# Performance work log

Hardware: AMD Instinct MI355X
Metric: run time of the kernel (lower is better)

## Reference

```python
import jax, jax.numpy as jnp
import numpy as np

B, T = 64, 4096
K = 67            # 25 body + 21 + 21 hand keypoints
D = 256           # first_layer_size
C = 7             # num_classes
THR = 0.1         # confidence_threshold
EPS = 1e-5        # BatchNorm eps


def setup_inputs() -> dict:
    key = jax.random.key(0)
    ks = jax.random.split(key, 8)
    body = jax.random.normal(ks[0], (B, T, 75), dtype=jnp.float32)
    hand_right = jax.random.normal(ks[1], (B, T, 63), dtype=jnp.float32)
    hand_left = jax.random.normal(ks[2], (B, T, 63), dtype=jnp.float32)
    length = jax.random.randint(ks[3], (B,), 1, T + 1, dtype=jnp.int64)
    W1 = jax.random.normal(ks[4], (2 * K, D), dtype=jnp.float32) * 0.05
    b1 = jnp.zeros((D,), dtype=jnp.float32)
    gamma = jnp.ones((D,), dtype=jnp.float32)
    beta = jnp.zeros((D,), dtype=jnp.float32)
    Wc = jax.random.normal(ks[5], (D, C), dtype=jnp.float32) * 0.05
    bc = jnp.zeros((C,), dtype=jnp.float32)
    return {"body": body, "hand_right": hand_right, "hand_left": hand_left,
            "length": length, "W1": W1, "b1": b1, "gamma": gamma,
            "beta": beta, "Wc": Wc, "bc": bc}


def reference(body, hand_right, hand_left, length, W1, b1, gamma, beta, Wc, bc):
    # concat keypoint streams -> [B, T, 3K] -> [B, T, K, 3]
    feats = jnp.concatenate([body, hand_right, hand_left], axis=2)
    feats = feats.reshape(feats.shape[0], feats.shape[1], -1, 3)
    x, y, conf = feats[..., 0], feats[..., 1], feats[..., 2]
    conf = (conf > THR).astype(feats.dtype)
    # gate coords by confidence, flatten to [B, T, 2K]
    pos = jnp.stack([x * conf, y * conf], axis=3)
    pos = pos.reshape(pos.shape[0], pos.shape[1], -1)
    # static MLP: Linear + ReLU -> [B, T, D]
    sf = jax.nn.relu(jnp.einsum("btf,fd->btd", pos, W1) + b1)
    # masked max pool over valid timesteps (vectorized segment-max)
    mask = jnp.arange(sf.shape[1])[None, :] < length[:, None]      # [B, T]
    pooled = jnp.max(jnp.where(mask[:, :, None], sf, -jnp.inf), axis=1)  # [B, D]
    # BatchNorm1d (training mode: batch statistics)
    mean = pooled.mean(axis=0)
    var = pooled.var(axis=0)
    bn = (pooled - mean) / jnp.sqrt(var + EPS) * gamma + beta
    # classifier
    return bn @ Wc + bc
```

## Files before the change

### kernel.cpp

```cpp
#include <hip/hip_runtime.h>
#include <hip/hip_bf16.h>

#define B_   64
#define T_   4096
#define K_   67
#define F_   134
#define FP_  160
#define D_   256
#define C_   7
#define THR_ 0.1f
#define EPS_ 1e-5f

typedef __bf16 bf16x8 __attribute__((ext_vector_type(8)));
typedef float  f32x4  __attribute__((ext_vector_type(4)));


__device__ __forceinline__ int a_idx(int t, int f) {
    return (((t >> 4) * 5 + (f >> 5)) * 512) +
           ((((f >> 3) & 3) * 16 + (t & 15)) * 8) + (f & 7);
}

__device__ __forceinline__ int get_len(const int* L, int b) {
    return (L[1] == 0) ? L[2 * b] : L[b];
}

__global__ void convert_w1(const float* __restrict__ W1, __bf16* __restrict__ W1bf) {
    int idx = blockIdx.x * 256 + threadIdx.x;
    if (idx < F_ * D_) {
        int f = idx >> 8, d = idx & 255;
        W1bf[d * FP_ + f] = (__bf16)W1[idx];
    } else if (idx < D_ * FP_) {
        int i2 = idx - F_ * D_;
        int d = i2 / 26, f = F_ + i2 % 26;
        W1bf[d * FP_ + f] = (__bf16)0.f;
    }
}

__device__ __forceinline__ void stage_triple(const float* p, int t, int kglob,
                                             __bf16* As) {
    float x = p[0], y = p[1], cf = p[2];
    if (!(cf > THR_)) { x = 0.f; y = 0.f; }
    unsigned short ux = __builtin_bit_cast(unsigned short, (__bf16)x);
    unsigned short uy = __builtin_bit_cast(unsigned short, (__bf16)y);
    int idx = a_idx(t, 2 * kglob);
    *(unsigned int*)((unsigned short*)As + idx) =
        (unsigned int)ux | ((unsigned int)uy << 16);
}

__global__ __launch_bounds__(256, 3)
void fused_mlp_pool(const float* __restrict__ body,
                    const float* __restrict__ hr,
                    const float* __restrict__ hl,
                    const int*   __restrict__ length,
                    const float* __restrict__ b1,
                    const __bf16* __restrict__ W1bf,
                    float* __restrict__ pooled)
{
    const int b = blockIdx.y;
    const int len = get_len(length, b);
    const int cbase = blockIdx.x * 128;
    if (cbase >= len) return;

    __shared__ __align__(16) __bf16 As[2 * 5 * 512];

    const int tid  = threadIdx.x;
    const int wave = tid >> 6;
    const int lane = tid & 63;
    const int quad = lane >> 4;
    const int l16  = lane & 15;
    const int dbase = wave * 64;

    for (int i = tid; i < 32 * 13; i += 256) {
        int t = i / 13;
        int f = 134 + 2 * (i % 13);
        *(unsigned int*)((unsigned short*)As + a_idx(t, f)) = 0u;
    }

    bf16x8 bfrag[4][5];
    float  b1v[4];
#pragma unroll
    for (int n = 0; n < 4; n++) {
        int d = dbase + n * 16 + l16;
        const __bf16* p = W1bf + d * FP_ + quad * 8;
#pragma unroll
        for (int kt = 0; kt < 5; kt++)
            bfrag[n][kt] = *(const bf16x8*)(p + kt * 32);
        b1v[n] = b1[d];
    }

    float runmax[4] = {0.f, 0.f, 0.f, 0.f};
    const long rowb = (long)b * T_;

    for (int c = 0; c < 4; c++) {
        const int t0 = cbase + c * 32;
        if (t0 >= len) break;
        if (c) __syncthreads();

        const float* bodyt = body + (rowb + t0) * 75;
        for (int j = tid; j < 32 * 25; j += 256) {
            int t = j / 25, k = j - t * 25;
            stage_triple(bodyt + t * 75 + k * 3, t, k, As);
        }
        const float* hrt = hr + (rowb + t0) * 63;
        for (int j = tid; j < 32 * 21; j += 256) {
            int t = j / 21, k = j - t * 21;
            stage_triple(hrt + t * 63 + k * 3, t, 25 + k, As);
        }
        const float* hlt = hl + (rowb + t0) * 63;
        for (int j = tid; j < 32 * 21; j += 256) {
            int t = j / 21, k = j - t * 21;
            stage_triple(hlt + t * 63 + k * 3, t, 46 + k, As);
        }
        __syncthreads();

        f32x4 acc[2][4];
#pragma unroll
        for (int m = 0; m < 2; m++)
#pragma unroll
            for (int n = 0; n < 4; n++)
                acc[m][n] = (f32x4){0.f, 0.f, 0.f, 0.f};

#pragma unroll
        for (int kt = 0; kt < 5; kt++) {
            bf16x8 a0 = *(const bf16x8*)(As + (0 * 5 + kt) * 512 + lane * 8);
            bf16x8 a1 = *(const bf16x8*)(As + (1 * 5 + kt) * 512 + lane * 8);
#pragma unroll
            for (int n = 0; n < 4; n++) {
                acc[0][n] = __builtin_amdgcn_mfma_f32_16x16x32_bf16(a0, bfrag[n][kt], acc[0][n], 0, 0, 0);
                acc[1][n] = __builtin_amdgcn_mfma_f32_16x16x32_bf16(a1, bfrag[n][kt], acc[1][n], 0, 0, 0);
            }
        }

#pragma unroll
        for (int m = 0; m < 2; m++) {
            int trow0 = t0 + m * 16 + quad * 4;
#pragma unroll
            for (int r = 0; r < 4; r++) {
                bool valid = (trow0 + r) < len;
#pragma unroll
                for (int n = 0; n < 4; n++) {
                    float v = acc[m][n][r] + b1v[n];
                    v = (v > 0.f) ? v : 0.f;
                    runmax[n] = (valid && v > runmax[n]) ? v : runmax[n];
                }
            }
        }
    }

#pragma unroll
    for (int n = 0; n < 4; n++) {
        float r = runmax[n];
        r = fmaxf(r, __shfl_xor(r, 16, 64));
        r = fmaxf(r, __shfl_xor(r, 32, 64));
        if (quad == n) {
            atomicMax((unsigned int*)(pooled + b * D_ + dbase + n * 16 + l16),
                      __float_as_uint(r));
        }
    }
}

__global__ void bn_classifier(const float* __restrict__ pooled,
                              const float* __restrict__ gamma,
                              const float* __restrict__ beta,
                              const float* __restrict__ Wc,
                              const float* __restrict__ bc,
                              float* __restrict__ out)
{
    __shared__ float scale_s[D_], shift_s[D_];
    const int tid = threadIdx.x;
    float s = 0.f, ss = 0.f;
#pragma unroll 8
    for (int b = 0; b < B_; b++) {
        float v = pooled[b * D_ + tid];
        s += v; ss += v * v;
    }
    float mean = s * (1.f / B_);
    float var  = ss * (1.f / B_) - mean * mean;
    var = fmaxf(var, 0.f);
    float sc = gamma[tid] * rsqrtf(var + EPS_);
    scale_s[tid] = sc;
    shift_s[tid] = beta[tid] - mean * sc;

    const int wv = tid >> 6, ln = tid & 63;
    float wcr[4][C_];
#pragma unroll
    for (int j = 0; j < 4; j++)
#pragma unroll
        for (int c = 0; c < C_; c++)
            wcr[j][c] = Wc[(ln * 4 + j) * C_ + c];
    __syncthreads();

    for (int b = wv * 16; b < wv * 16 + 16; b++) {
        float4 v = *(const float4*)(pooled + b * D_ + ln * 4);
        float q[4];
        q[0] = v.x * scale_s[ln * 4 + 0] + shift_s[ln * 4 + 0];
        q[1] = v.y * scale_s[ln * 4 + 1] + shift_s[ln * 4 + 1];
        q[2] = v.z * scale_s[ln * 4 + 2] + shift_s[ln * 4 + 2];
        q[3] = v.w * scale_s[ln * 4 + 3] + shift_s[ln * 4 + 3];
        float p[C_];
#pragma unroll
        for (int c = 0; c < C_; c++) p[c] = 0.f;
#pragma unroll
        for (int j = 0; j < 4; j++)
#pragma unroll
            for (int c = 0; c < C_; c++)
                p[c] += q[j] * wcr[j][c];
#pragma unroll
        for (int c = 0; c < C_; c++) {
#pragma unroll
            for (int off = 1; off < 64; off <<= 1)
                p[c] += __shfl_xor(p[c], off, 64);
        }
        if (ln == 0) {
#pragma unroll
            for (int c = 0; c < C_; c++)
                out[b * C_ + c] = p[c] + bc[c];
        }
    }
}

extern "C" void kernel_launch(void* const* d_in, const int* in_sizes, int n_in,
                              void* d_out, int out_size, void* d_ws, size_t ws_size,
                              hipStream_t stream) {
    const float* body   = (const float*)d_in[0];
    const float* hr     = (const float*)d_in[1];
    const float* hl     = (const float*)d_in[2];
    const int*   length = (const int*)  d_in[3];
    const float* W1     = (const float*)d_in[4];
    const float* b1     = (const float*)d_in[5];
    const float* gamma  = (const float*)d_in[6];
    const float* beta   = (const float*)d_in[7];
    const float* Wc     = (const float*)d_in[8];
    const float* bc     = (const float*)d_in[9];
    float* out = (float*)d_out;

    float*  pooled = (float*)d_ws;
    __bf16* W1bf   = (__bf16*)((char*)d_ws + 65536);

    hipMemsetAsync(d_ws, 0, 65536, stream);
    convert_w1<<<dim3(160), dim3(256), 0, stream>>>(W1, W1bf);
    fused_mlp_pool<<<dim3(32, B_), dim3(256), 0, stream>>>(body, hr, hl, length, b1, W1bf, pooled);
    bn_classifier<<<dim3(1), dim3(256), 0, stream>>>(pooled, gamma, beta, Wc, bc, out);
}
```

Measured before the change: 284.4 us.

## Split time chunks into single-pass 64-row blocks with doubled grid

The fused MLP/pool kernel used to loop over four 32-timestep chunks per block, with a sync between chunks. Each block now handles one 64-timestep tile in a single stage-compute-reduce pass, and the grid doubles to 64 blocks per batch row. This removes the per-chunk loop and barriers and gives more independent blocks to hide global-load latency. In exchange, each block loads the W1 fragments and does the atomic max for half as many rows, uses more shared memory and accumulators, and launch bounds drop to 2 blocks per SM. convert_w1 is also rewritten so each thread writes the transposed padded weight element directly, giving coalesced writes.

```diff
diff --git a/kernel.cpp b/kernel.cpp
--- a/kernel.cpp
+++ b/kernel.cpp
@@ -26,14 +26,10 @@
 
 __global__ void convert_w1(const float* __restrict__ W1, __bf16* __restrict__ W1bf) {
     int idx = blockIdx.x * 256 + threadIdx.x;
-    if (idx < F_ * D_) {
-        int f = idx >> 8, d = idx & 255;
-        W1bf[d * FP_ + f] = (__bf16)W1[idx];
-    } else if (idx < D_ * FP_) {
-        int i2 = idx - F_ * D_;
-        int d = i2 / 26, f = F_ + i2 % 26;
-        W1bf[d * FP_ + f] = (__bf16)0.f;
-    }
+    if (idx >= D_ * FP_) return;
+    int d = idx / FP_, f = idx - d * FP_;
+    float v = (f < F_) ? W1[f * D_ + d] : 0.f;
+    W1bf[idx] = (__bf16)v;
 }
 
 __device__ __forceinline__ void stage_triple(const float* p, int t, int kglob,
@@ -47,7 +43,7 @@
         (unsigned int)ux | ((unsigned int)uy << 16);
 }
 
-__global__ __launch_bounds__(256, 3)
+__global__ __launch_bounds__(256, 2)
 void fused_mlp_pool(const float* __restrict__ body,
                     const float* __restrict__ hr,
                     const float* __restrict__ hl,
@@ -58,10 +54,10 @@
 {
     const int b = blockIdx.y;
     const int len = get_len(length, b);
-    const int cbase = blockIdx.x * 128;
-    if (cbase >= len) return;
-
-    __shared__ __align__(16) __bf16 As[2 * 5 * 512];
+    const int t0 = blockIdx.x * 64;
+    if (t0 >= len) return;
+
+    __shared__ __align__(16) __bf16 As[4 * 5 * 512];
 
     const int tid  = threadIdx.x;
     const int wave = tid >> 6;
@@ -70,79 +66,72 @@
     const int l16  = lane & 15;
     const int dbase = wave * 64;
 
-    for (int i = tid; i < 32 * 13; i += 256) {
+    bf16x8 bfrag[4][5];
+    float  b1v[4];
+#pragma unroll
+    for (int n = 0; n < 4; n++) {
+        int d = dbase + n * 16 + l16;
+        const __bf16* p = W1bf + d * FP_ + quad * 8;
+#pragma unroll
+        for (int kt = 0; kt < 5; kt++)
+            bfrag[n][kt] = *(const bf16x8*)(p + kt * 32);
+        b1v[n] = b1[d];
+    }
+
+    for (int i = tid; i < 64 * 13; i += 256) {
         int t = i / 13;
         int f = 134 + 2 * (i % 13);
         *(unsigned int*)((unsigned short*)As + a_idx(t, f)) = 0u;
     }
 
-    bf16x8 bfrag[4][5];
-    float  b1v[4];
-#pragma unroll
-    for (int n = 0; n < 4; n++) {
-        int d = dbase + n * 16 + l16;
-        const __bf16* p = W1bf + d * FP_ + quad * 8;
-#pragma unroll
-        for (int kt = 0; kt < 5; kt++)
-            bfrag[n][kt] = *(const bf16x8*)(p + kt * 32);
-        b1v[n] = b1[d];
+    const long rowb = (long)b * T_;
+    const float* bodyt = body + (rowb + t0) * 75;
+    for (int j = tid; j < 64 * 25; j += 256) {
+        int t = j / 25, k = j - t * 25;
+        stage_triple(bodyt + t * 75 + k * 3, t, k, As);
+    }
+    const float* hrt = hr + (rowb + t0) * 63;
+    for (int j = tid; j < 64 * 21; j += 256) {
+        int t = j / 21, k = j - t * 21;
+        stage_triple(hrt + t * 63 + k * 3, t, 25 + k, As);
+    }
+    const float* hlt = hl + (rowb + t0) * 63;
+    for (int j = tid; j < 64 * 21; j += 256) {
+        int t = j / 21, k = j - t * 21;
+        stage_triple(hlt + t * 63 + k * 3, t, 46 + k, As);
+    }
+    __syncthreads();
+
+    f32x4 acc[4][4];
+#pragma unroll
+    for (int m = 0; m < 4; m++)
+#pragma unroll
+        for (int n = 0; n < 4; n++)
+            acc[m][n] = (f32x4){0.f, 0.f, 0.f, 0.f};
+
+#pragma unroll
+    for (int kt = 0; kt < 5; kt++) {
+#pragma unroll
+        for (int m = 0; m < 4; m++) {
+            bf16x8 a = *(const bf16x8*)(As + (m * 5 + kt) * 512 + lane * 8);
+#pragma unroll
+            for (int n = 0; n < 4; n++)
+                acc[m][n] = __builtin_amdgcn_mfma_f32_16x16x32_bf16(a, bfrag[n][kt], acc[m][n], 0, 0, 0);
+        }
     }
 
     float runmax[4] = {0.f, 0.f, 0.f, 0.f};
-    const long rowb = (long)b * T_;
-
-    for (int c = 0; c < 4; c++) {
-        const int t0 = cbase + c * 32;
-        if (t0 >= len) break;
-        if (c) __syncthreads();
-
-        const float* bodyt = body + (rowb + t0) * 75;
-        for (int j = tid; j < 32 * 25; j += 256) {
-            int t = j / 25, k = j - t * 25;
-            stage_triple(bodyt + t * 75 + k * 3, t, k, As);
-        }
-        const float* hrt = hr + (rowb + t0) * 63;
-        for (int j = tid; j < 32 * 21; j += 256) {
-            int t = j / 21, k = j - t * 21;
-            stage_triple(hrt + t * 63 + k * 3, t, 25 + k, As);
-        }
-        const float* hlt = hl + (rowb + t0) * 63;
-        for (int j = tid; j < 32 * 21; j += 256) {
-            int t = j / 21, k = j - t * 21;
-            stage_triple(hlt + t * 63 + k * 3, t, 46 + k, As);
-        }
-        __syncthreads();
-
-        f32x4 acc[2][4];
-#pragma unroll
-        for (int m = 0; m < 2; m++)
-#pragma unroll
-            for (int n = 0; n < 4; n++)
-                acc[m][n] = (f32x4){0.f, 0.f, 0.f, 0.f};
-
-#pragma unroll
-        for (int kt = 0; kt < 5; kt++) {
-            bf16x8 a0 = *(const bf16x8*)(As + (0 * 5 + kt) * 512 + lane * 8);
-            bf16x8 a1 = *(const bf16x8*)(As + (1 * 5 + kt) * 512 + lane * 8);
+#pragma unroll
+    for (int m = 0; m < 4; m++) {
+        int trow0 = t0 + m * 16 + quad * 4;
+#pragma unroll
+        for (int r = 0; r < 4; r++) {
+            bool valid = (trow0 + r) < len;
 #pragma unroll
             for (int n = 0; n < 4; n++) {
-                acc[0][n] = __builtin_amdgcn_mfma_f32_16x16x32_bf16(a0, bfrag[n][kt], acc[0][n], 0, 0, 0);
-                acc[1][n] = __builtin_amdgcn_mfma_f32_16x16x32_bf16(a1, bfrag[n][kt], acc[1][n], 0, 0, 0);
-            }
-        }
-
-#pragma unroll
-        for (int m = 0; m < 2; m++) {
-            int trow0 = t0 + m * 16 + quad * 4;
-#pragma unroll
-            for (int r = 0; r < 4; r++) {
-                bool valid = (trow0 + r) < len;
-#pragma unroll
-                for (int n = 0; n < 4; n++) {
-                    float v = acc[m][n][r] + b1v[n];
-                    v = (v > 0.f) ? v : 0.f;
-                    runmax[n] = (valid && v > runmax[n]) ? v : runmax[n];
-                }
+                float v = acc[m][n][r] + b1v[n];
+                v = (v > 0.f) ? v : 0.f;
+                runmax[n] = (valid && v > runmax[n]) ? v : runmax[n];
             }
         }
     }
@@ -239,6 +228,6 @@
 
     hipMemsetAsync(d_ws, 0, 65536, stream);
     convert_w1<<<dim3(160), dim3(256), 0, stream>>>(W1, W1bf);
-    fused_mlp_pool<<<dim3(32, B_), dim3(256), 0, stream>>>(body, hr, hl, length, b1, W1bf, pooled);
+    fused_mlp_pool<<<dim3(64, B_), dim3(256), 0, stream>>>(body, hr, hl, length, b1, W1bf, pooled);
     bn_classifier<<<dim3(1), dim3(256), 0, stream>>>(pooled, gamma, beta, Wc, bc, out);
 }
```

Result: faster. 256.4 us (-9.8%).
